# Kernel tuning notes

Hardware: AMD Instinct MI355X
Metric: run time of the kernel (lower is better)

The kernel has to match this reference:

```python
import jax
import jax.numpy as jnp
from jax import lax
import numpy as np

S_DIM = 8
K = 2
TAU = 0.01
MAX_ITER = 100
TOL = 1e-3


def setup_inputs() -> dict:
    key = jax.random.key(0)
    s = jax.random.normal(key, (4_000_000, S_DIM), dtype=jnp.float32)
    return {"s": s}


def _compute_threshold(s, k, tau):
    # init: (k+1)-th largest element per row, matching sorted_s[:, -k-1]
    sorted_s = jnp.sort(s, axis=-1)
    theta0 = sorted_s[:, -k - 1][:, None]  # (B, 1)

    def step(carry, _):
        theta, done = carry
        m = jax.nn.sigmoid((s - theta) / tau)                 # (B, S)
        f = m.sum(axis=-1, keepdims=True) - k                 # (B, 1)
        # torch breaks BEFORE the update when mean(f) < tol
        new_done = done | (jnp.mean(f) < TOL)
        df = -(1.0 / tau) * (m * (1.0 - m)).sum(axis=-1, keepdims=True)
        theta_new = jnp.where(new_done, theta, theta - f / df)
        return (theta_new, new_done), None

    (theta, _), _ = lax.scan(step, (theta0, jnp.array(False)), None, length=MAX_ITER)
    return theta


def reference(s) -> jnp.ndarray:
    theta = _compute_threshold(s, K, TAU)
    return jax.nn.sigmoid((s - theta) / TAU)
```

## Files before the change

kernel.cpp:

```cpp
#include <hip/hip_runtime.h>


__global__ __launch_bounds__(256) void smooth_topk_kernel(
    const float* __restrict__ s, float* __restrict__ out, int nhalf) {
  int gid = blockIdx.x * blockDim.x + threadIdx.x;
  if (gid >= nhalf) return;

  const float C = 144.26950408889634f;

  float4 v4 = reinterpret_cast<const float4*>(s)[gid];
  float v0 = v4.x * C, v1 = v4.y * C, v2 = v4.z * C, v3 = v4.w * C;

  float a = fmaxf(v0, v1), b = fminf(v0, v1);
  float c = fmaxf(v2, v3), d = fminf(v2, v3);
  float mn = fminf(a, c);
  float p1 = fmaxf(a, c);
  float p2 = fmaxf(mn, fmaxf(b, d));
  float p3 = __builtin_amdgcn_fmed3f(b, d, mn);

  float q1 = __shfl_xor(p1, 1, 64);
  float q2 = __shfl_xor(p2, 1, 64);
  float q3 = __shfl_xor(p3, 1, 64);

  float t2 = fmaxf(fminf(p1, q1), fmaxf(p2, q2));
  float t3 = fmaxf(fmaxf(fminf(p2, q1), fminf(p1, q2)), fmaxf(p3, q3));

  float phi = 0.5f * (t2 + t3);
  const float lo = t3 - 4.33f;
  const float hi = t2 + 4.33f;

#pragma unroll
  for (int it = 0; it < 3; ++it) {
    float e0 = __builtin_amdgcn_exp2f(phi - v0);
    float e1 = __builtin_amdgcn_exp2f(phi - v1);
    float e2 = __builtin_amdgcn_exp2f(phi - v2);
    float e3 = __builtin_amdgcn_exp2f(phi - v3);
    float m0 = __builtin_amdgcn_rcpf(1.0f + e0);
    float m1 = __builtin_amdgcn_rcpf(1.0f + e1);
    float m2 = __builtin_amdgcn_rcpf(1.0f + e2);
    float m3 = __builtin_amdgcn_rcpf(1.0f + e3);
    float fh = (m0 + m1) + (m2 + m3);
    float gh = fmaf(m0, 1.0f - m0, fmaf(m1, 1.0f - m1,
               fmaf(m2, 1.0f - m2, m3 * (1.0f - m3))));
    float f = (fh + __shfl_xor(fh, 1, 64)) - 2.0f;
    float g = gh + __shfl_xor(gh, 1, 64);
    float step = f * 1.4426950408889634f * __builtin_amdgcn_rcpf(fmaxf(g, 1e-12f));
    phi = fminf(fmaxf(phi + step, lo), hi);
  }

  float4 o;
  o.x = __builtin_amdgcn_rcpf(1.0f + __builtin_amdgcn_exp2f(phi - v0));
  o.y = __builtin_amdgcn_rcpf(1.0f + __builtin_amdgcn_exp2f(phi - v1));
  o.z = __builtin_amdgcn_rcpf(1.0f + __builtin_amdgcn_exp2f(phi - v2));
  o.w = __builtin_amdgcn_rcpf(1.0f + __builtin_amdgcn_exp2f(phi - v3));
  reinterpret_cast<float4*>(out)[gid] = o;
}

extern "C" void kernel_launch(void* const* d_in, const int* in_sizes, int n_in,
                              void* d_out, int out_size, void* d_ws, size_t ws_size,
                              hipStream_t stream) {
  const float* s = (const float*)d_in[0];
  float* out = (float*)d_out;
  int nhalf = in_sizes[0] / 4;
  int block = 256;
  int grid = (nhalf + block - 1) / block;
  smooth_topk_kernel<<<grid, block, 0, stream>>>(s, out, nhalf);
}
```

Before: 210.4 us.

## Process two row-halves per thread, fold last Newton step into first-order output

Each thread now handles two float4 items (strided by n) with non-temporal loads and stores. The Newton loop drops from three iterations to two, and the third step's theta update is applied to the output through a first-order Taylor correction instead of recomputing exp and rcp. This cuts transcendental work and adds per-thread ILP. It changes the numerics slightly and relies on the input size dividing evenly into two halves.

Measured after the change: 208.4 us. No clear change (-0.9%).

```diff
diff --git a/kernel.cpp b/kernel.cpp
--- a/kernel.cpp
+++ b/kernel.cpp
@@ -1,59 +1,100 @@
 #include <hip/hip_runtime.h>
 
 
+typedef float f32x4 __attribute__((ext_vector_type(4)));
+
 __global__ __launch_bounds__(256) void smooth_topk_kernel(
-    const float* __restrict__ s, float* __restrict__ out, int nhalf) {
+    const float* __restrict__ s, float* __restrict__ out, int n) {
+  constexpr int ITEMS = 2;
   int gid = blockIdx.x * blockDim.x + threadIdx.x;
-  if (gid >= nhalf) return;
+  if (gid >= n) return;
 
   const float C = 144.26950408889634f;
+  const float LOG2E = 1.4426950408889634f;
+  const float LN2 = 0.6931471805599453f;
 
-  float4 v4 = reinterpret_cast<const float4*>(s)[gid];
-  float v0 = v4.x * C, v1 = v4.y * C, v2 = v4.z * C, v3 = v4.w * C;
-
-  float a = fmaxf(v0, v1), b = fminf(v0, v1);
-  float c = fmaxf(v2, v3), d = fminf(v2, v3);
-  float mn = fminf(a, c);
-  float p1 = fmaxf(a, c);
-  float p2 = fmaxf(mn, fmaxf(b, d));
-  float p3 = __builtin_amdgcn_fmed3f(b, d, mn);
-
-  float q1 = __shfl_xor(p1, 1, 64);
-  float q2 = __shfl_xor(p2, 1, 64);
-  float q3 = __shfl_xor(p3, 1, 64);
-
-  float t2 = fmaxf(fminf(p1, q1), fmaxf(p2, q2));
-  float t3 = fmaxf(fmaxf(fminf(p2, q1), fminf(p1, q2)), fmaxf(p3, q3));
-
-  float phi = 0.5f * (t2 + t3);
-  const float lo = t3 - 4.33f;
-  const float hi = t2 + 4.33f;
+  float v0[ITEMS], v1[ITEMS], v2[ITEMS], v3[ITEMS];
+  float phi[ITEMS], lo[ITEMS], hi[ITEMS];
 
 #pragma unroll
-  for (int it = 0; it < 3; ++it) {
-    float e0 = __builtin_amdgcn_exp2f(phi - v0);
-    float e1 = __builtin_amdgcn_exp2f(phi - v1);
-    float e2 = __builtin_amdgcn_exp2f(phi - v2);
-    float e3 = __builtin_amdgcn_exp2f(phi - v3);
+  for (int u = 0; u < ITEMS; ++u) {
+    f32x4 v4 = __builtin_nontemporal_load(
+        reinterpret_cast<const f32x4*>(s) + (gid + u * n));
+    v0[u] = v4.x * C;
+    v1[u] = v4.y * C;
+    v2[u] = v4.z * C;
+    v3[u] = v4.w * C;
+
+    float a = fmaxf(v0[u], v1[u]), b = fminf(v0[u], v1[u]);
+    float c = fmaxf(v2[u], v3[u]), d = fminf(v2[u], v3[u]);
+    float mn = fminf(a, c);
+    float p1 = fmaxf(a, c);
+    float p2 = fmaxf(mn, fmaxf(b, d));
+    float p3 = __builtin_amdgcn_fmed3f(b, d, mn);
+
+    float q1 = __shfl_xor(p1, 1, 64);
+    float q2 = __shfl_xor(p2, 1, 64);
+    float q3 = __shfl_xor(p3, 1, 64);
+
+    float t2 = fmaxf(fminf(p1, q1), fmaxf(p2, q2));
+    float t3 = fmaxf(fmaxf(fminf(p2, q1), fminf(p1, q2)), fmaxf(p3, q3));
+
+    phi[u] = 0.5f * (t2 + t3);
+    lo[u] = t3 - 4.33f;
+    hi[u] = t2 + 4.33f;
+  }
+
+#pragma unroll
+  for (int it = 0; it < 2; ++it) {
+#pragma unroll
+    for (int u = 0; u < ITEMS; ++u) {
+      float e0 = __builtin_amdgcn_exp2f(phi[u] - v0[u]);
+      float e1 = __builtin_amdgcn_exp2f(phi[u] - v1[u]);
+      float e2 = __builtin_amdgcn_exp2f(phi[u] - v2[u]);
+      float e3 = __builtin_amdgcn_exp2f(phi[u] - v3[u]);
+      float m0 = __builtin_amdgcn_rcpf(1.0f + e0);
+      float m1 = __builtin_amdgcn_rcpf(1.0f + e1);
+      float m2 = __builtin_amdgcn_rcpf(1.0f + e2);
+      float m3 = __builtin_amdgcn_rcpf(1.0f + e3);
+      float fh = (m0 + m1) + (m2 + m3);
+      float gh = fmaf(m0, 1.0f - m0, fmaf(m1, 1.0f - m1,
+                 fmaf(m2, 1.0f - m2, m3 * (1.0f - m3))));
+      float f = (fh + __shfl_xor(fh, 1, 64)) - 2.0f;
+      float g = gh + __shfl_xor(gh, 1, 64);
+      float step = f * LOG2E * __builtin_amdgcn_rcpf(fmaxf(g, 1e-12f));
+      phi[u] = fminf(fmaxf(phi[u] + step, lo[u]), hi[u]);
+    }
+  }
+
+#pragma unroll
+  for (int u = 0; u < ITEMS; ++u) {
+    float e0 = __builtin_amdgcn_exp2f(phi[u] - v0[u]);
+    float e1 = __builtin_amdgcn_exp2f(phi[u] - v1[u]);
+    float e2 = __builtin_amdgcn_exp2f(phi[u] - v2[u]);
+    float e3 = __builtin_amdgcn_exp2f(phi[u] - v3[u]);
     float m0 = __builtin_amdgcn_rcpf(1.0f + e0);
     float m1 = __builtin_amdgcn_rcpf(1.0f + e1);
     float m2 = __builtin_amdgcn_rcpf(1.0f + e2);
     float m3 = __builtin_amdgcn_rcpf(1.0f + e3);
+    float c0 = m0 * (1.0f - m0);
+    float c1 = m1 * (1.0f - m1);
+    float c2 = m2 * (1.0f - m2);
+    float c3 = m3 * (1.0f - m3);
     float fh = (m0 + m1) + (m2 + m3);
-    float gh = fmaf(m0, 1.0f - m0, fmaf(m1, 1.0f - m1,
-               fmaf(m2, 1.0f - m2, m3 * (1.0f - m3))));
+    float gh = (c0 + c1) + (c2 + c3);
     float f = (fh + __shfl_xor(fh, 1, 64)) - 2.0f;
     float g = gh + __shfl_xor(gh, 1, 64);
-    float step = f * 1.4426950408889634f * __builtin_amdgcn_rcpf(fmaxf(g, 1e-12f));
-    phi = fminf(fmaxf(phi + step, lo), hi);
+    float step = f * LOG2E * __builtin_amdgcn_rcpf(fmaxf(g, 1e-12f));
+    float phin = fminf(fmaxf(phi[u] + step, lo[u]), hi[u]);
+    float w = (phin - phi[u]) * LN2;
+
+    f32x4 o;
+    o.x = fmaf(-w, c0, m0);
+    o.y = fmaf(-w, c1, m1);
+    o.z = fmaf(-w, c2, m2);
+    o.w = fmaf(-w, c3, m3);
+    __builtin_nontemporal_store(o, reinterpret_cast<f32x4*>(out) + (gid + u * n));
   }
-
-  float4 o;
-  o.x = __builtin_amdgcn_rcpf(1.0f + __builtin_amdgcn_exp2f(phi - v0));
-  o.y = __builtin_amdgcn_rcpf(1.0f + __builtin_amdgcn_exp2f(phi - v1));
-  o.z = __builtin_amdgcn_rcpf(1.0f + __builtin_amdgcn_exp2f(phi - v2));
-  o.w = __builtin_amdgcn_rcpf(1.0f + __builtin_amdgcn_exp2f(phi - v3));
-  reinterpret_cast<float4*>(out)[gid] = o;
 }
 
 extern "C" void kernel_launch(void* const* d_in, const int* in_sizes, int n_in,
@@ -62,7 +103,8 @@
   const float* s = (const float*)d_in[0];
   float* out = (float*)d_out;
   int nhalf = in_sizes[0] / 4;
+  int n = nhalf >> 1;
   int block = 256;
-  int grid = (nhalf + block - 1) / block;
-  smooth_topk_kernel<<<grid, block, 0, stream>>>(s, out, nhalf);
+  int grid = (n + block - 1) / block;
+  smooth_topk_kernel<<<grid, block, 0, stream>>>(s, out, n);
 }
```

## Grid-stride loop with prefetch, nontemporal I/O, and first-order final sigmoid

Applied to the files above, without the earlier changes.

Turns the kernel into a grid-stride loop with about ten float4 items per thread, prefetching the next input vector while computing the current one. Loads and stores use nontemporal hints. The third Newton iteration's sigmoid values are reused for the output through a first-order Taylor correction (m - w*m*(1-m)) instead of recomputing exp and rcp a fourth time. This removes one transcendental pass and per-thread launch overhead, at the cost of a small approximation in the output and fewer waves in flight.

After: 211.8 us. Within noise of the previous version (+0.7%).

```diff
diff --git a/kernel.cpp b/kernel.cpp
--- a/kernel.cpp
+++ b/kernel.cpp
@@ -1,59 +1,97 @@
 #include <hip/hip_runtime.h>
 
 
+typedef float f32x4 __attribute__((ext_vector_type(4)));
+
 __global__ __launch_bounds__(256) void smooth_topk_kernel(
-    const float* __restrict__ s, float* __restrict__ out, int nhalf) {
-  int gid = blockIdx.x * blockDim.x + threadIdx.x;
-  if (gid >= nhalf) return;
+    const float* __restrict__ s, float* __restrict__ out, int n) {
+  const int stride = gridDim.x * blockDim.x;
+  int idx = blockIdx.x * blockDim.x + threadIdx.x;
 
   const float C = 144.26950408889634f;
+  const float LOG2E = 1.4426950408889634f;
+  const float LN2 = 0.6931471805599453f;
 
-  float4 v4 = reinterpret_cast<const float4*>(s)[gid];
-  float v0 = v4.x * C, v1 = v4.y * C, v2 = v4.z * C, v3 = v4.w * C;
+  f32x4 vnext = {0.0f, 0.0f, 0.0f, 0.0f};
+  if (idx < n)
+    vnext = __builtin_nontemporal_load(reinterpret_cast<const f32x4*>(s) + idx);
 
-  float a = fmaxf(v0, v1), b = fminf(v0, v1);
-  float c = fmaxf(v2, v3), d = fminf(v2, v3);
-  float mn = fminf(a, c);
-  float p1 = fmaxf(a, c);
-  float p2 = fmaxf(mn, fmaxf(b, d));
-  float p3 = __builtin_amdgcn_fmed3f(b, d, mn);
+  while (idx < n) {
+    f32x4 v4 = vnext;
+    int idx2 = idx + stride;
+    if (idx2 < n)
+      vnext = __builtin_nontemporal_load(reinterpret_cast<const f32x4*>(s) + idx2);
 
-  float q1 = __shfl_xor(p1, 1, 64);
-  float q2 = __shfl_xor(p2, 1, 64);
-  float q3 = __shfl_xor(p3, 1, 64);
+    float v0 = v4.x * C, v1 = v4.y * C, v2 = v4.z * C, v3 = v4.w * C;
 
-  float t2 = fmaxf(fminf(p1, q1), fmaxf(p2, q2));
-  float t3 = fmaxf(fmaxf(fminf(p2, q1), fminf(p1, q2)), fmaxf(p3, q3));
+    float a = fmaxf(v0, v1), b = fminf(v0, v1);
+    float c = fmaxf(v2, v3), d = fminf(v2, v3);
+    float mn = fminf(a, c);
+    float p1 = fmaxf(a, c);
+    float p2 = fmaxf(mn, fmaxf(b, d));
+    float p3 = __builtin_amdgcn_fmed3f(b, d, mn);
 
-  float phi = 0.5f * (t2 + t3);
-  const float lo = t3 - 4.33f;
-  const float hi = t2 + 4.33f;
+    float q1 = __shfl_xor(p1, 1, 64);
+    float q2 = __shfl_xor(p2, 1, 64);
+    float q3 = __shfl_xor(p3, 1, 64);
+
+    float t2 = fmaxf(fminf(p1, q1), fmaxf(p2, q2));
+    float t3 = fmaxf(fmaxf(fminf(p2, q1), fminf(p1, q2)), fmaxf(p3, q3));
+
+    float phi = 0.5f * (t2 + t3);
+    const float lo = t3 - 4.33f;
+    const float hi = t2 + 4.33f;
 
 #pragma unroll
-  for (int it = 0; it < 3; ++it) {
-    float e0 = __builtin_amdgcn_exp2f(phi - v0);
-    float e1 = __builtin_amdgcn_exp2f(phi - v1);
-    float e2 = __builtin_amdgcn_exp2f(phi - v2);
-    float e3 = __builtin_amdgcn_exp2f(phi - v3);
-    float m0 = __builtin_amdgcn_rcpf(1.0f + e0);
-    float m1 = __builtin_amdgcn_rcpf(1.0f + e1);
-    float m2 = __builtin_amdgcn_rcpf(1.0f + e2);
-    float m3 = __builtin_amdgcn_rcpf(1.0f + e3);
-    float fh = (m0 + m1) + (m2 + m3);
-    float gh = fmaf(m0, 1.0f - m0, fmaf(m1, 1.0f - m1,
-               fmaf(m2, 1.0f - m2, m3 * (1.0f - m3))));
-    float f = (fh + __shfl_xor(fh, 1, 64)) - 2.0f;
-    float g = gh + __shfl_xor(gh, 1, 64);
-    float step = f * 1.4426950408889634f * __builtin_amdgcn_rcpf(fmaxf(g, 1e-12f));
-    phi = fminf(fmaxf(phi + step, lo), hi);
+    for (int it = 0; it < 2; ++it) {
+      float e0 = __builtin_amdgcn_exp2f(phi - v0);
+      float e1 = __builtin_amdgcn_exp2f(phi - v1);
+      float e2 = __builtin_amdgcn_exp2f(phi - v2);
+      float e3 = __builtin_amdgcn_exp2f(phi - v3);
+      float m0 = __builtin_amdgcn_rcpf(1.0f + e0);
+      float m1 = __builtin_amdgcn_rcpf(1.0f + e1);
+      float m2 = __builtin_amdgcn_rcpf(1.0f + e2);
+      float m3 = __builtin_amdgcn_rcpf(1.0f + e3);
+      float fh = (m0 + m1) + (m2 + m3);
+      float gh = fmaf(m0, 1.0f - m0, fmaf(m1, 1.0f - m1,
+                 fmaf(m2, 1.0f - m2, m3 * (1.0f - m3))));
+      float f = (fh + __shfl_xor(fh, 1, 64)) - 2.0f;
+      float g = gh + __shfl_xor(gh, 1, 64);
+      float step = f * LOG2E * __builtin_amdgcn_rcpf(fmaxf(g, 1e-12f));
+      phi = fminf(fmaxf(phi + step, lo), hi);
+    }
+
+    {
+      float e0 = __builtin_amdgcn_exp2f(phi - v0);
+      float e1 = __builtin_amdgcn_exp2f(phi - v1);
+      float e2 = __builtin_amdgcn_exp2f(phi - v2);
+      float e3 = __builtin_amdgcn_exp2f(phi - v3);
+      float m0 = __builtin_amdgcn_rcpf(1.0f + e0);
+      float m1 = __builtin_amdgcn_rcpf(1.0f + e1);
+      float m2 = __builtin_amdgcn_rcpf(1.0f + e2);
+      float m3 = __builtin_amdgcn_rcpf(1.0f + e3);
+      float c0 = m0 * (1.0f - m0);
+      float c1 = m1 * (1.0f - m1);
+      float c2 = m2 * (1.0f - m2);
+      float c3 = m3 * (1.0f - m3);
+      float fh = (m0 + m1) + (m2 + m3);
+      float gh = (c0 + c1) + (c2 + c3);
+      float f = (fh + __shfl_xor(fh, 1, 64)) - 2.0f;
+      float g = gh + __shfl_xor(gh, 1, 64);
+      float step = f * LOG2E * __builtin_amdgcn_rcpf(fmaxf(g, 1e-12f));
+      float phin = fminf(fmaxf(phi + step, lo), hi);
+      float w = (phin - phi) * LN2;
+
+      f32x4 o;
+      o.x = fmaf(-w, c0, m0);
+      o.y = fmaf(-w, c1, m1);
+      o.z = fmaf(-w, c2, m2);
+      o.w = fmaf(-w, c3, m3);
+      __builtin_nontemporal_store(o, reinterpret_cast<f32x4*>(out) + idx);
+    }
+
+    idx = idx2;
   }
-
-  float4 o;
-  o.x = __builtin_amdgcn_rcpf(1.0f + __builtin_amdgcn_exp2f(phi - v0));
-  o.y = __builtin_amdgcn_rcpf(1.0f + __builtin_amdgcn_exp2f(phi - v1));
-  o.z = __builtin_amdgcn_rcpf(1.0f + __builtin_amdgcn_exp2f(phi - v2));
-  o.w = __builtin_amdgcn_rcpf(1.0f + __builtin_amdgcn_exp2f(phi - v3));
-  reinterpret_cast<float4*>(out)[gid] = o;
 }
 
 extern "C" void kernel_launch(void* const* d_in, const int* in_sizes, int n_in,
@@ -63,6 +101,9 @@
   float* out = (float*)d_out;
   int nhalf = in_sizes[0] / 4;
   int block = 256;
-  int grid = (nhalf + block - 1) / block;
+  int grid = (nhalf + block * 10 - 1) / (block * 10);
+  int max_grid = (nhalf + block - 1) / block;
+  if (grid > max_grid) grid = max_grid;
+  if (grid < 1) grid = 1;
   smooth_topk_kernel<<<grid, block, 0, stream>>>(s, out, nhalf);
 }
```
